# Performance work log

Hardware: AMD Instinct MI355X
Metric: run time of the kernel (lower is better)

The kernel has to match this reference:

```python
import jax, jax.numpy as jnp
import numpy as np

V, B, T, D, H = 32000, 64, 256, 512, 1024


def setup_inputs() -> dict:
    key = jax.random.key(0)
    ks = jax.random.split(key, 8)
    s = lambda i, shape: (jax.random.normal(ks[i], shape, jnp.float32) * 0.02)
    return {
        "y": jax.random.randint(ks[0], (B, T), 0, V),
        "hidden": jnp.zeros((B, H), jnp.float32),
        "emb_table": s(1, (V, D)),
        "Wx": s(2, (D, 3 * H)),
        "Wh": s(3, (H, 3 * H)),
        "bx": jnp.zeros((3 * H,), jnp.float32),
        "bh": jnp.zeros((3 * H,), jnp.float32),
        "W_out": s(4, (H, D)),
        "b_out": jnp.zeros((D,), jnp.float32),
    }


def _gru_step(h, x, Wx, Wh, bx, bh):
    # PyTorch GRUCell semantics: r,z gates, candidate n with r gating the
    # recurrent contribution (including its bias term).
    gx = x @ Wx + bx          # [B, 3H]
    gh = h @ Wh + bh          # [B, 3H]
    xr, xz, xn = jnp.split(gx, 3, axis=-1)
    hr, hz, hn = jnp.split(gh, 3, axis=-1)
    r = jax.nn.sigmoid(xr + hr)
    z = jax.nn.sigmoid(xz + hz)
    n = jnp.tanh(xn + r * hn)
    return (1.0 - z) * n + z * h


def reference(y, hidden, emb_table, Wx, Wh, bx, bh, W_out, b_out):
    emb = emb_table[y]                       # [B, T, D] token embedding lookup

    def step(h, x_t):                        # x_t: [B, D]
        h2 = _gru_step(h, x_t, Wx, Wh, bx, bh)
        return h2, h2

    _, outs = jax.lax.scan(step, hidden, jnp.swapaxes(emb, 0, 1))  # [T, B, H]
    out = jnp.swapaxes(outs, 0, 1)           # [B, T, H] decoder hiddens
    logits = jnp.tanh(out @ W_out + b_out)   # [B, T, D]; dropout_rate=0 -> identity
    return logits
```

## Files before the change

kernel.cpp:

```cpp
#include <hip/hip_runtime.h>
#include <stdint.h>

typedef unsigned short u16;
typedef unsigned int u32;
typedef __attribute__((ext_vector_type(4))) unsigned int u32x4;
typedef __attribute__((ext_vector_type(4))) float f32x4;
typedef __attribute__((ext_vector_type(8))) __bf16 bf16x8;

#define MFMA16(a, b, c) __builtin_amdgcn_mfma_f32_16x16x32_bf16((a), (b), (c), 0, 0, 0)

__device__ __forceinline__ u16 f2b(float f) {
  union { float f; unsigned u; } v; v.f = f;
  unsigned r = v.u + 0x7FFFu + ((v.u >> 16) & 1u);
  return (u16)(r >> 16);
}
__device__ __forceinline__ float b2f(u16 h) {
  union { unsigned u; float f; } v; v.u = ((unsigned)h) << 16;
  return v.f;
}
__device__ __forceinline__ float sigm(float x) { return 1.0f / (1.0f + __expf(-x)); }
__device__ __forceinline__ float tanh_fast(float x) {
  x = fminf(fmaxf(x, -15.0f), 15.0f);
  float t = __expf(2.0f * x);
  return (t - 1.0f) / (t + 1.0f);
}

template <int OFF>
__device__ __forceinline__ u32x4 ld16_sc(const void* p) {
  u32x4 r;
  asm volatile("global_load_dwordx4 %0, %1, off offset:%2 sc0 sc1"
               : "=v"(r) : "v"(p), "i"(OFF));
  return r;
}
__device__ __forceinline__ void st16_sc(void* p, u32x4 v) {
  asm volatile("global_store_dwordx4 %0, %1, off sc0 sc1"
               :: "v"(p), "v"(v) : "memory");
}

__device__ __forceinline__ void gld_lds16(const void* g, void* l) {
  __builtin_amdgcn_global_load_lds(
      (const __attribute__((address_space(1))) void*)(g),
      (__attribute__((address_space(3))) void*)(l), 16, 0, 0);
}

__global__ __launch_bounds__(256) void prep_all(
    const float* __restrict__ Wx, const float* __restrict__ Wh,
    const float* __restrict__ Wout, const int* __restrict__ y,
    const float* __restrict__ emb, const float* __restrict__ hidden,
    u16* __restrict__ wx_t, u16* __restrict__ wh_t, u16* __restrict__ wo_t,
    u16* __restrict__ aemb, u16* __restrict__ hbuf) {
  __shared__ float tile[32][33];
  const int b = blockIdx.x, tid = threadIdx.x;
  const int tx = tid & 31, ty = tid >> 5;

  const float* src = nullptr; u16* dst = nullptr; int R = 0, C = 0, tb = 0;
  if (b < 1536)      { src = Wx;   dst = wx_t; R = 512;  C = 3072; tb = b; }
  else if (b < 4608) { src = Wh;   dst = wh_t; R = 1024; C = 3072; tb = b - 1536; }
  else if (b < 5120) { src = Wout; dst = wo_t; R = 1024; C = 512;  tb = b - 4608; }

  if (src) {
    const int xt = C >> 5;
    const int c0 = (tb % xt) * 32, r0 = (tb / xt) * 32;
    for (int i = ty; i < 32; i += 8)
      tile[i][tx] = src[(size_t)(r0 + i) * C + (c0 + tx)];
    __syncthreads();
    for (int i = ty; i < 32; i += 8)
      dst[(size_t)(c0 + i) * R + (r0 + tx)] = f2b(tile[tx][i]);
    return;
  }
  if (b < 13312) {
    const int idx = (b - 5120) * 256 + tid;
    const int m = idx >> 7, d0 = (idx & 127) << 2;
    const float4 v = *reinterpret_cast<const float4*>(emb + (size_t)y[m] * 512 + d0);
    ushort4 o;
    o.x = f2b(v.x); o.y = f2b(v.y); o.z = f2b(v.z); o.w = f2b(v.w);
    *reinterpret_cast<ushort4*>(aemb + (size_t)m * 512 + d0) = o;
    return;
  }
  if (b < 13568) {
    const int i = (b - 13312) * 256 + tid;
    const int bb = i >> 10, n = i & 1023;
    const int r = bb >> 4, ii = bb & 15, g = n >> 4, j = n & 15;
    u16 v = f2b(hidden[(size_t)bb * 1024 + n]);
    if (!(j & 1)) v |= 1;
    hbuf[((size_t)r * 64 + g) * 256 + ii * 16 + j] = v;
    return;
  }
  {
    const size_t idx = (size_t)(b - 13568) * 256 + tid;
    u32x4 z = {0, 0, 0, 0};
    *(u32x4*)(hbuf + 65536 + idx * 8) = z;
  }
}

template <int EPI, int ALAYOUT>
__global__ __launch_bounds__(256, 2) void gemm_bt(
    const u16* __restrict__ A, const u16* __restrict__ Bt,
    const float* __restrict__ bias, void* __restrict__ Cout,
    int M, int N, int K) {
  __shared__ u16 As[4096], Bs[4096];
  const int tid = threadIdx.x, lane = tid & 63, w = tid >> 6;
  const int wm = w >> 1, wn = w & 1, c = lane & 15, hq = lane >> 4;
  const int m0 = blockIdx.y * 128, n0 = blockIdx.x * 128;
  f32x4 acc[4][4] = {};

  const int r0_ = tid >> 2, ko0 = (tid & 3) << 3;
  const int r1_ = (256 + tid) >> 2, ko1 = ((256 + tid) & 3) << 3;

  for (int k0 = 0; k0 < K; k0 += 32) {
    const u16 *ga0, *ga1;
    if (ALAYOUT == 0) {
      ga0 = A + (size_t)(m0 + r0_) * K + k0 + ko0;
      ga1 = A + (size_t)(m0 + r1_) * K + k0 + ko1;
    } else {
      const int ma = m0 + r0_, ka = k0 + ko0, mb = m0 + r1_, kb = k0 + ko1;
      ga0 = A + ((((size_t)(ma >> 6) + 1) * 4 + ((ma >> 4) & 3)) * 64 +
                 (ka >> 4)) * 256 + (ma & 15) * 16 + (ka & 15);
      ga1 = A + ((((size_t)(mb >> 6) + 1) * 4 + ((mb >> 4) & 3)) * 64 +
                 (kb >> 4)) * 256 + (mb & 15) * 16 + (kb & 15);
    }
    const u16* gb0 = Bt + (size_t)(n0 + r0_) * K + k0 + ko0;
    const u16* gb1 = Bt + (size_t)(n0 + r1_) * K + k0 + ko1;
    __syncthreads();
    gld_lds16(ga0, (char*)As + tid * 16);
    gld_lds16(ga1, (char*)As + 4096 + tid * 16);
    gld_lds16(gb0, (char*)Bs + tid * 16);
    gld_lds16(gb1, (char*)Bs + 4096 + tid * 16);
    __syncthreads();
    u32x4 af[4], bf[4];
#pragma unroll
    for (int i = 0; i < 4; ++i) {
      af[i] = *(const u32x4*)(As + (wm * 64 + i * 16 + c) * 32 + hq * 8);
      bf[i] = *(const u32x4*)(Bs + (wn * 64 + i * 16 + c) * 32 + hq * 8);
    }
#pragma unroll
    for (int mi = 0; mi < 4; ++mi)
#pragma unroll
      for (int ni = 0; ni < 4; ++ni)
        acc[mi][ni] = MFMA16(__builtin_bit_cast(bf16x8, af[mi]),
                             __builtin_bit_cast(bf16x8, bf[ni]), acc[mi][ni]);
  }

#pragma unroll
  for (int ni = 0; ni < 4; ++ni) {
    const int col = n0 + wn * 64 + ni * 16 + c;
    const float bv = bias[col];
#pragma unroll
    for (int mi = 0; mi < 4; ++mi) {
#pragma unroll
      for (int i = 0; i < 4; ++i) {
        const int m = m0 + wm * 64 + mi * 16 + hq * 4 + i;
        const float v = acc[mi][ni][i] + bv;
        if (EPI == 0) {
          const int dr = (m & 255) * 64 + (m >> 8);
          ((u16*)Cout)[(size_t)dr * N + col] = f2b(v);
        } else {
          const int dr = (m & 63) * 256 + (m >> 6);
          ((float*)Cout)[(size_t)dr * N + col] = tanh_fast(v);
        }
      }
    }
  }
}

__global__ __launch_bounds__(320, 1) void scan_kernel(
    const u16* __restrict__ wh_t,
    const float* __restrict__ bh,
    const float* __restrict__ h0,
    const u16* __restrict__ gx,
    u16* __restrict__ hbuf) {
  __shared__ u16 whs[96 * 512];
  __shared__ float red[2][4][3][256];
  __shared__ __align__(16) u16 htile[16][16];
  const int g = blockIdx.x >> 2, r = blockIdx.x & 3;
  const int tid = threadIdx.x, lane = tid & 63, s = tid >> 6;
  const int c = lane & 15, hq = lane >> 4;
  const int gcol = g * 16 + c;
  const int row0 = r * 16;

  for (int fb = s; fb < 96; fb += 5) {
    const int ss = fb / 24, kk = (fb % 24) / 3, ct = fb % 3;
    const int n = ct * 1024 + g * 16 + c;
    const int k = ss * 256 + kk * 32 + hq * 8;
    *(u32x4*)(whs + fb * 512 + lane * 8) =
        *(const u32x4*)(wh_t + (size_t)n * 1024 + k);
  }
  float bhv[3], hprev[4];
  u16 gxr[4][3];
  if (s == 4) {
#pragma unroll
    for (int ct = 0; ct < 3; ++ct) bhv[ct] = bh[ct * 1024 + gcol];
#pragma unroll
    for (int i = 0; i < 4; ++i)
      hprev[i] = h0[(size_t)(row0 + hq * 4 + i) * 1024 + gcol];
    const u16* gp = gx + gcol;
#pragma unroll
    for (int i = 0; i < 4; ++i) {
      const int b = row0 + hq * 4 + i;
      gxr[i][0] = gp[(size_t)b * 3072];
      gxr[i][1] = gp[(size_t)b * 3072 + 1024];
      gxr[i][2] = gp[(size_t)b * 3072 + 2048];
    }
  }
  __syncthreads();

  for (int t = 0; t < 256; ++t) {
    if (s < 4) {
      const u16* slotBase = hbuf + ((size_t)t * 4 + r) * 16384;

      if (t > 0) {
        const u16* pp = slotBase + (s * 16 + (lane & 15)) * 256;
        u32 v0, v1;
        if (lane < 16) {
          asm volatile("global_load_ushort %0, %1, off sc0 sc1" : "=v"(v0) : "v"(pp));
          asm volatile("global_load_ushort %0, %1, off sc0 sc1" : "=v"(v1) : "v"(pp));
          while (true) {
            asm volatile("s_waitcnt vmcnt(1)" : "+v"(v0));
            if (!__ballot(!(v0 & 1))) break;
            asm volatile("global_load_ushort %0, %1, off sc0 sc1" : "=v"(v0) : "v"(pp));
            asm volatile("s_waitcnt vmcnt(1)" : "+v"(v1));
            if (!__ballot(!(v1 & 1))) break;
            asm volatile("global_load_ushort %0, %1, off sc0 sc1" : "=v"(v1) : "v"(pp));
          }
        }
      }

      u32x4 af[8];
      const u16* ap0 = slotBase + (s * 16 + (hq >> 1)) * 256 + c * 16 + (hq & 1) * 8;
      const u16* ap1 = ap0 + 2048;
      while (true) {
        af[0] = ld16_sc<0>(ap0);    af[1] = ld16_sc<1024>(ap0);
        af[2] = ld16_sc<2048>(ap0); af[3] = ld16_sc<3072>(ap0);
        af[4] = ld16_sc<0>(ap1);    af[5] = ld16_sc<1024>(ap1);
        af[6] = ld16_sc<2048>(ap1); af[7] = ld16_sc<3072>(ap1);
        asm volatile("s_waitcnt vmcnt(0)" ::: "memory");
        __builtin_amdgcn_sched_barrier(0);
        u32 bad = 0;
#pragma unroll
        for (int q = 0; q < 8; ++q)
#pragma unroll
          for (int e = 0; e < 4; ++e) bad |= (~af[q][e]) & 1u;
        if (!__ballot(bad != 0)) break;
      }

      f32x4 acc[3] = {};
#pragma unroll
      for (int kk = 0; kk < 8; ++kk) {
        const int fb = (s * 8 + kk) * 3;
        const u32x4 b0 = *(const u32x4*)(whs + (fb + 0) * 512 + lane * 8);
        const u32x4 b1 = *(const u32x4*)(whs + (fb + 1) * 512 + lane * 8);
        const u32x4 b2 = *(const u32x4*)(whs + (fb + 2) * 512 + lane * 8);
        const bf16x8 a = __builtin_bit_cast(bf16x8, af[kk]);
        acc[0] = MFMA16(a, __builtin_bit_cast(bf16x8, b0), acc[0]);
        acc[1] = MFMA16(a, __builtin_bit_cast(bf16x8, b1), acc[1]);
        acc[2] = MFMA16(a, __builtin_bit_cast(bf16x8, b2), acc[2]);
      }
#pragma unroll
      for (int ct = 0; ct < 3; ++ct)
        *(f32x4*)&red[t & 1][s][ct][lane * 4] = acc[ct];
    }
    __syncthreads();

    if (s == 4) {
      f32x4 a0 = {}, a1 = {}, a2 = {};
#pragma unroll
      for (int j = 0; j < 4; ++j) {
        a0 += *(const f32x4*)&red[t & 1][j][0][lane * 4];
        a1 += *(const f32x4*)&red[t & 1][j][1][lane * 4];
        a2 += *(const f32x4*)&red[t & 1][j][2][lane * 4];
      }
#pragma unroll
      for (int i = 0; i < 4; ++i) {
        const float xr = b2f(gxr[i][0]);
        const float xz = b2f(gxr[i][1]);
        const float xn = b2f(gxr[i][2]);
        const float rr = sigm(xr + a0[i] + bhv[0]);
        const float zz = sigm(xz + a1[i] + bhv[1]);
        const float nn = tanh_fast(xn + rr * (a2[i] + bhv[2]));
        const float hnew = (1.0f - zz) * nn + zz * hprev[i];
        hprev[i] = hnew;
        u16 hb = f2b(hnew);
        if (!(c & 1)) hb |= 1;
        htile[hq * 4 + i][c] = hb;
      }
      asm volatile("s_waitcnt lgkmcnt(0)" ::: "memory");
      __builtin_amdgcn_sched_barrier(0);
      if (lane < 32) {
        const u32x4 hv = *(const u32x4*)((const u16*)htile + lane * 8);
        st16_sc(hbuf + ((size_t)(t + 1) * 4 + r) * 16384 + g * 256 + lane * 8, hv);
      }
      if (t < 255) {
        const u16* gp = gx + (size_t)(t + 1) * 64 * 3072 + gcol;
#pragma unroll
        for (int i = 0; i < 4; ++i) {
          const int b = row0 + hq * 4 + i;
          gxr[i][0] = gp[(size_t)b * 3072];
          gxr[i][1] = gp[(size_t)b * 3072 + 1024];
          gxr[i][2] = gp[(size_t)b * 3072 + 2048];
        }
      }
    }
  }
}

extern "C" void kernel_launch(void* const* d_in, const int* in_sizes, int n_in,
                              void* d_out, int out_size, void* d_ws, size_t ws_size,
                              hipStream_t stream) {
  (void)in_sizes; (void)n_in; (void)out_size; (void)ws_size;
  const int* y = (const int*)d_in[0];
  const float* hidden = (const float*)d_in[1];
  const float* emb = (const float*)d_in[2];
  const float* Wx = (const float*)d_in[3];
  const float* Wh = (const float*)d_in[4];
  const float* bx = (const float*)d_in[5];
  const float* bh = (const float*)d_in[6];
  const float* Wout = (const float*)d_in[7];
  const float* bout = (const float*)d_in[8];

  char* p = (char*)d_ws;
  u16* wx_t = (u16*)p; p += (size_t)3072 * 512 * 2;
  u16* wh_t = (u16*)p; p += (size_t)3072 * 1024 * 2;
  u16* wo_t = (u16*)p; p += (size_t)512 * 1024 * 2;
  u16* aemb = (u16*)p; p += (size_t)16384 * 512 * 2;
  u16* gx   = (u16*)p; p += (size_t)16384 * 3072 * 2;
  u16* hbuf = (u16*)p; p += (size_t)257 * 4 * 64 * 256 * 2;

  prep_all<<<dim3(21760), dim3(256), 0, stream>>>(Wx, Wh, Wout, y, emb, hidden,
                                                  wx_t, wh_t, wo_t, aemb, hbuf);
  gemm_bt<0, 0><<<dim3(24, 128), dim3(256), 0, stream>>>(aemb, wx_t, bx, (void*)gx,
                                                         16384, 3072, 512);
  scan_kernel<<<dim3(256), dim3(320), 0, stream>>>(wh_t, bh, hidden, gx, hbuf);
  gemm_bt<1, 1><<<dim3(4, 128), dim3(256), 0, stream>>>(hbuf, wo_t, bout,
                                                        d_out, 16384, 512, 1024);
}
```

Baseline: 873.0 us.

## Fuse input projection GEMM into recurrent scan kernel

Removes the separate x@Wx GEMM and its large bf16 gx intermediate. Each scan step now loads the time-major embedding rows and multiplies them by register-resident Wx fragments inside the scan kernel. The n-gate's input and recurrent parts go to separate accumulators so the r gating still applies only to the recurrent part. This saves a kernel launch and a large write/read round trip, but puts extra MFMA work and embedding loads on the serial critical path of every timestep.

Result: slower. 923.1 us (+5.7%).

```diff
diff --git a/kernel.cpp b/kernel.cpp
--- a/kernel.cpp
+++ b/kernel.cpp
@@ -74,7 +74,8 @@
     const float4 v = *reinterpret_cast<const float4*>(emb + (size_t)y[m] * 512 + d0);
     ushort4 o;
     o.x = f2b(v.x); o.y = f2b(v.y); o.z = f2b(v.z); o.w = f2b(v.w);
-    *reinterpret_cast<ushort4*>(aemb + (size_t)m * 512 + d0) = o;
+    const int dr = (m & 255) * 64 + (m >> 8);
+    *reinterpret_cast<ushort4*>(aemb + (size_t)dr * 512 + d0) = o;
     return;
   }
   if (b < 13568) {
@@ -93,10 +94,9 @@
   }
 }
 
-template <int EPI, int ALAYOUT>
-__global__ __launch_bounds__(256, 2) void gemm_bt(
+__global__ __launch_bounds__(256, 2) void gemm_out(
     const u16* __restrict__ A, const u16* __restrict__ Bt,
-    const float* __restrict__ bias, void* __restrict__ Cout,
+    const float* __restrict__ bias, float* __restrict__ Cout,
     int M, int N, int K) {
   __shared__ u16 As[4096], Bs[4096];
   const int tid = threadIdx.x, lane = tid & 63, w = tid >> 6;
@@ -108,17 +108,11 @@
   const int r1_ = (256 + tid) >> 2, ko1 = ((256 + tid) & 3) << 3;
 
   for (int k0 = 0; k0 < K; k0 += 32) {
-    const u16 *ga0, *ga1;
-    if (ALAYOUT == 0) {
-      ga0 = A + (size_t)(m0 + r0_) * K + k0 + ko0;
-      ga1 = A + (size_t)(m0 + r1_) * K + k0 + ko1;
-    } else {
-      const int ma = m0 + r0_, ka = k0 + ko0, mb = m0 + r1_, kb = k0 + ko1;
-      ga0 = A + ((((size_t)(ma >> 6) + 1) * 4 + ((ma >> 4) & 3)) * 64 +
-                 (ka >> 4)) * 256 + (ma & 15) * 16 + (ka & 15);
-      ga1 = A + ((((size_t)(mb >> 6) + 1) * 4 + ((mb >> 4) & 3)) * 64 +
-                 (kb >> 4)) * 256 + (mb & 15) * 16 + (kb & 15);
-    }
+    const int ma = m0 + r0_, ka = k0 + ko0, mb = m0 + r1_, kb = k0 + ko1;
+    const u16* ga0 = A + ((((size_t)(ma >> 6) + 1) * 4 + ((ma >> 4) & 3)) * 64 +
+                          (ka >> 4)) * 256 + (ma & 15) * 16 + (ka & 15);
+    const u16* ga1 = A + ((((size_t)(mb >> 6) + 1) * 4 + ((mb >> 4) & 3)) * 64 +
+                          (kb >> 4)) * 256 + (mb & 15) * 16 + (kb & 15);
     const u16* gb0 = Bt + (size_t)(n0 + r0_) * K + k0 + ko0;
     const u16* gb1 = Bt + (size_t)(n0 + r1_) * K + k0 + ko1;
     __syncthreads();
@@ -150,14 +144,8 @@
 #pragma unroll
       for (int i = 0; i < 4; ++i) {
         const int m = m0 + wm * 64 + mi * 16 + hq * 4 + i;
-        const float v = acc[mi][ni][i] + bv;
-        if (EPI == 0) {
-          const int dr = (m & 255) * 64 + (m >> 8);
-          ((u16*)Cout)[(size_t)dr * N + col] = f2b(v);
-        } else {
-          const int dr = (m & 63) * 256 + (m >> 6);
-          ((float*)Cout)[(size_t)dr * N + col] = tanh_fast(v);
-        }
+        const int dr = (m & 63) * 256 + (m >> 6);
+        Cout[(size_t)dr * N + col] = tanh_fast(acc[mi][ni][i] + bv);
       }
     }
   }
@@ -165,12 +153,14 @@
 
 __global__ __launch_bounds__(320, 1) void scan_kernel(
     const u16* __restrict__ wh_t,
+    const u16* __restrict__ wx_t,
     const float* __restrict__ bh,
+    const float* __restrict__ bx,
     const float* __restrict__ h0,
-    const u16* __restrict__ gx,
+    const u16* __restrict__ aemb,
     u16* __restrict__ hbuf) {
   __shared__ u16 whs[96 * 512];
-  __shared__ float red[2][4][3][256];
+  __shared__ float red[2][4][4][256];
   __shared__ __align__(16) u16 htile[16][16];
   const int g = blockIdx.x >> 2, r = blockIdx.x & 3;
   const int tid = threadIdx.x, lane = tid & 63, s = tid >> 6;
@@ -185,22 +175,24 @@
     *(u32x4*)(whs + fb * 512 + lane * 8) =
         *(const u32x4*)(wh_t + (size_t)n * 1024 + k);
   }
-  float bhv[3], hprev[4];
-  u16 gxr[4][3];
+  u32x4 wxf[12];
+  if (s < 4) {
+#pragma unroll
+    for (int kk = 0; kk < 4; ++kk)
+#pragma unroll
+      for (int ct = 0; ct < 3; ++ct)
+        wxf[kk * 3 + ct] = *(const u32x4*)(
+            wx_t + ((size_t)(ct * 1024 + g * 16 + c)) * 512 + s * 128 + kk * 32 + hq * 8);
+  }
+  float bxr = 0, bxz = 0, bxn = 0, bhr = 0, bhz = 0, bhn = 0;
+  float hprev[4];
   if (s == 4) {
-#pragma unroll
-    for (int ct = 0; ct < 3; ++ct) bhv[ct] = bh[ct * 1024 + gcol];
+    bxr = bx[gcol];          bhr = bh[gcol];
+    bxz = bx[1024 + gcol];   bhz = bh[1024 + gcol];
+    bxn = bx[2048 + gcol];   bhn = bh[2048 + gcol];
 #pragma unroll
     for (int i = 0; i < 4; ++i)
       hprev[i] = h0[(size_t)(row0 + hq * 4 + i) * 1024 + gcol];
-    const u16* gp = gx + gcol;
-#pragma unroll
-    for (int i = 0; i < 4; ++i) {
-      const int b = row0 + hq * 4 + i;
-      gxr[i][0] = gp[(size_t)b * 3072];
-      gxr[i][1] = gp[(size_t)b * 3072 + 1024];
-      gxr[i][2] = gp[(size_t)b * 3072 + 2048];
-    }
   }
   __syncthreads();
 
@@ -225,6 +217,13 @@
         }
       }
 
+      u32x4 ef[4];
+      {
+        const u16* ep = aemb + ((size_t)t * 64 + row0 + c) * 512 + s * 128 + hq * 8;
+        ef[0] = ld16_sc<0>(ep);   ef[1] = ld16_sc<64>(ep);
+        ef[2] = ld16_sc<128>(ep); ef[3] = ld16_sc<192>(ep);
+      }
+
       u32x4 af[8];
       const u16* ap0 = slotBase + (s * 16 + (hq >> 1)) * 256 + c * 16 + (hq & 1) * 8;
       const u16* ap1 = ap0 + 2048;
@@ -243,7 +242,14 @@
         if (!__ballot(bad != 0)) break;
       }
 
-      f32x4 acc[3] = {};
+      f32x4 acc[4] = {};
+#pragma unroll
+      for (int kk = 0; kk < 4; ++kk) {
+        const bf16x8 a = __builtin_bit_cast(bf16x8, ef[kk]);
+        acc[0] = MFMA16(a, __builtin_bit_cast(bf16x8, wxf[kk * 3 + 0]), acc[0]);
+        acc[1] = MFMA16(a, __builtin_bit_cast(bf16x8, wxf[kk * 3 + 1]), acc[1]);
+        acc[2] = MFMA16(a, __builtin_bit_cast(bf16x8, wxf[kk * 3 + 2]), acc[2]);
+      }
 #pragma unroll
       for (int kk = 0; kk < 8; ++kk) {
         const int fb = (s * 8 + kk) * 3;
@@ -253,30 +259,28 @@
         const bf16x8 a = __builtin_bit_cast(bf16x8, af[kk]);
         acc[0] = MFMA16(a, __builtin_bit_cast(bf16x8, b0), acc[0]);
         acc[1] = MFMA16(a, __builtin_bit_cast(bf16x8, b1), acc[1]);
-        acc[2] = MFMA16(a, __builtin_bit_cast(bf16x8, b2), acc[2]);
-      }
-#pragma unroll
-      for (int ct = 0; ct < 3; ++ct)
+        acc[3] = MFMA16(a, __builtin_bit_cast(bf16x8, b2), acc[3]);
+      }
+#pragma unroll
+      for (int ct = 0; ct < 4; ++ct)
         *(f32x4*)&red[t & 1][s][ct][lane * 4] = acc[ct];
     }
     __syncthreads();
 
     if (s == 4) {
-      f32x4 a0 = {}, a1 = {}, a2 = {};
+      f32x4 a0 = {}, a1 = {}, a2e = {}, a2h = {};
 #pragma unroll
       for (int j = 0; j < 4; ++j) {
-        a0 += *(const f32x4*)&red[t & 1][j][0][lane * 4];
-        a1 += *(const f32x4*)&red[t & 1][j][1][lane * 4];
-        a2 += *(const f32x4*)&red[t & 1][j][2][lane * 4];
+        a0  += *(const f32x4*)&red[t & 1][j][0][lane * 4];
+        a1  += *(const f32x4*)&red[t & 1][j][1][lane * 4];
+        a2e += *(const f32x4*)&red[t & 1][j][2][lane * 4];
+        a2h += *(const f32x4*)&red[t & 1][j][3][lane * 4];
       }
 #pragma unroll
       for (int i = 0; i < 4; ++i) {
-        const float xr = b2f(gxr[i][0]);
-        const float xz = b2f(gxr[i][1]);
-        const float xn = b2f(gxr[i][2]);
-        const float rr = sigm(xr + a0[i] + bhv[0]);
-        const float zz = sigm(xz + a1[i] + bhv[1]);
-        const float nn = tanh_fast(xn + rr * (a2[i] + bhv[2]));
+        const float rr = sigm(a0[i] + bxr + bhr);
+        const float zz = sigm(a1[i] + bxz + bhz);
+        const float nn = tanh_fast(a2e[i] + bxn + rr * (a2h[i] + bhn));
         const float hnew = (1.0f - zz) * nn + zz * hprev[i];
         hprev[i] = hnew;
         u16 hb = f2b(hnew);
@@ -288,16 +292,6 @@
       if (lane < 32) {
         const u32x4 hv = *(const u32x4*)((const u16*)htile + lane * 8);
         st16_sc(hbuf + ((size_t)(t + 1) * 4 + r) * 16384 + g * 256 + lane * 8, hv);
-      }
-      if (t < 255) {
-        const u16* gp = gx + (size_t)(t + 1) * 64 * 3072 + gcol;
-#pragma unroll
-        for (int i = 0; i < 4; ++i) {
-          const int b = row0 + hq * 4 + i;
-          gxr[i][0] = gp[(size_t)b * 3072];
-          gxr[i][1] = gp[(size_t)b * 3072 + 1024];
-          gxr[i][2] = gp[(size_t)b * 3072 + 2048];
-        }
       }
     }
   }
@@ -322,14 +316,12 @@
   u16* wh_t = (u16*)p; p += (size_t)3072 * 1024 * 2;
   u16* wo_t = (u16*)p; p += (size_t)512 * 1024 * 2;
   u16* aemb = (u16*)p; p += (size_t)16384 * 512 * 2;
-  u16* gx   = (u16*)p; p += (size_t)16384 * 3072 * 2;
   u16* hbuf = (u16*)p; p += (size_t)257 * 4 * 64 * 256 * 2;
 
   prep_all<<<dim3(21760), dim3(256), 0, stream>>>(Wx, Wh, Wout, y, emb, hidden,
                                                   wx_t, wh_t, wo_t, aemb, hbuf);
-  gemm_bt<0, 0><<<dim3(24, 128), dim3(256), 0, stream>>>(aemb, wx_t, bx, (void*)gx,
-                                                         16384, 3072, 512);
-  scan_kernel<<<dim3(256), dim3(320), 0, stream>>>(wh_t, bh, hidden, gx, hbuf);
-  gemm_bt<1, 1><<<dim3(4, 128), dim3(256), 0, stream>>>(hbuf, wo_t, bout,
-                                                        d_out, 16384, 512, 1024);
-}
+  scan_kernel<<<dim3(256), dim3(320), 0, stream>>>(wh_t, wx_t, bh, bx, hidden,
+                                                   aemb, hbuf);
+  gemm_out<<<dim3(4, 128), dim3(256), 0, stream>>>(hbuf, wo_t, bout,
+                                                   (float*)d_out, 16384, 512, 1024);
+}
```
